# Performance work log

Hardware: AMD Instinct MI355X
Metric: run time of the kernel (lower is better)

## Reference

```python
import jax, jax.numpy as jnp
import numpy as np

B, H, S, D = 2, 8, 4096, 64
EPS = 1e-12  # torch F.normalize default eps

def _l2_normalize(x):
    n = jnp.linalg.norm(x, axis=-1, keepdims=True)
    return x / jnp.maximum(n, EPS)

def setup_inputs() -> dict:
    key = jax.random.key(0)
    kq, kk, kv, km = jax.random.split(key, 4)
    return {
        "query": jax.random.normal(kq, (B, H, S, D), dtype=jnp.float32),
        "key": jax.random.normal(kk, (B, H, S, D), dtype=jnp.float32),
        "value": jax.random.normal(kv, (B, H, S, D), dtype=jnp.float32),
        "mask": jax.random.randint(km, (B, 1, 1, S), 0, 2, dtype=jnp.int32),
    }

def reference(query, key, value, mask):
    q = _l2_normalize(query)
    k = _l2_normalize(key)
    # [B,H,S,S] cosine-similarity scores
    scores = jnp.einsum("bhqd,bhkd->bhqk", q, k)
    scores = jnp.where(mask == 0, jnp.float32(-1.0), scores)
    scores = (scores + 1.0) * 0.5  # map [-1,1] -> [0,1]; masked entries -> 0
    attention = scores / jnp.sum(scores, axis=-1, keepdims=True)
    return jnp.einsum("bhqk,bhkd->bhqd", attention, value)
```

## Files before the change

### kernel.cpp

```cpp
#include <hip/hip_runtime.h>


#define S 4096
#define D 64
#define BH 16
#define FSTRIDE 4352
#define NE 4225
#define NCHM 32
#define KSTR 36
#define QSTR 72
#define PSTR 8832
#define FTSTR 4224

typedef __attribute__((ext_vector_type(8))) short short8;
typedef __attribute__((ext_vector_type(4))) short short4v;
typedef __attribute__((ext_vector_type(4))) float f32x4;

__device__ __forceinline__ float bperm(float v, int srclane) {
    return __int_as_float(
        __builtin_amdgcn_ds_bpermute(srclane << 2, __float_as_int(v)));
}
__device__ __forceinline__ unsigned bf16h(float x) {
    unsigned u = __float_as_uint(x);
    u += 0x7FFF + ((u >> 16) & 1);
    return u >> 16;
}
__device__ __forceinline__ float bf16f(unsigned short h) {
    return __uint_as_float(((unsigned)h) << 16);
}

__global__ __launch_bounds__(256, 4) void k_moments(
    const float* __restrict__ K, const float* __restrict__ V,
    const int* __restrict__ mask, char* __restrict__ part)
{
    __shared__ unsigned short stag[8 * 64 * KSTR];
    __shared__ float sured[4 * 132];
    float* red0 = (float*)stag;
    float* red1 = red0 + 4096;

    const int tid  = threadIdx.x;
    const int lane = tid & 63;
    const int wave = tid >> 6;
    const int quad = lane >> 4;
    const int l15  = lane & 15;

    const int bh    = blockIdx.x >> 5;
    const int chunk = blockIdx.x & 31;
    const int row0  = chunk * 128 + wave * 32;

    const float* Kh = K + (size_t)bh * S * D;
    const float* Vh = V + (size_t)bh * S * D;
    const int*   mb = mask + (bh >> 3) * S;

    unsigned short* Kst = stag + wave * (64 * KSTR);
    unsigned short* Vst = stag + 4 * (64 * KSTR) + wave * (64 * KSTR);
    unsigned* KstW = (unsigned*)Kst;
    unsigned* VstW = (unsigned*)Vst;

    float4 s4 = {0.f, 0.f, 0.f, 0.f}, u4 = {0.f, 0.f, 0.f, 0.f};
    float nwp = 0.f;
    unsigned kprev[4], vprev[4];
    #pragma unroll
    for (int i = 0; i < 8; ++i) {
        const int key = 8 * quad + i;
        const int row = row0 + key;
        float4 kf = *(const float4*)(Kh + (size_t)row * D + 4 * l15);
        float4 vf = *(const float4*)(Vh + (size_t)row * D + 4 * l15);
        float ssp = kf.x * kf.x;
        ssp = fmaf(kf.y, kf.y, ssp);
        ssp = fmaf(kf.z, kf.z, ssp);
        ssp = fmaf(kf.w, kf.w, ssp);
        ssp += __shfl_xor(ssp, 1, 64);
        ssp += __shfl_xor(ssp, 2, 64);
        ssp += __shfl_xor(ssp, 4, 64);
        ssp += __shfl_xor(ssp, 8, 64);
        const float mj = (float)mb[row];
        nwp += mj;
        const float aj = mj * __builtin_amdgcn_rsqf(fmaxf(ssp, 1e-24f));
        float k0 = kf.x * aj, k1 = kf.y * aj, k2 = kf.z * aj, k3 = kf.w * aj;
        float v0 = vf.x * mj, v1 = vf.y * mj, v2 = vf.z * mj, v3 = vf.w * mj;
        s4.x += k0; s4.y += k1; s4.z += k2; s4.w += k3;
        u4.x += v0; u4.y += v1; u4.z += v2; u4.w += v3;
        unsigned kb0 = bf16h(k0), kb1 = bf16h(k1), kb2 = bf16h(k2), kb3 = bf16h(k3);
        unsigned vb0 = bf16h(v0), vb1 = bf16h(v1), vb2 = bf16h(v2), vb3 = bf16h(v3);
        if (i & 1) {
            const int base = 4 * quad + (i >> 1);
            KstW[(4 * l15 + 0) * 18 + base] = kprev[0] | (kb0 << 16);
            KstW[(4 * l15 + 1) * 18 + base] = kprev[1] | (kb1 << 16);
            KstW[(4 * l15 + 2) * 18 + base] = kprev[2] | (kb2 << 16);
            KstW[(4 * l15 + 3) * 18 + base] = kprev[3] | (kb3 << 16);
            VstW[(4 * l15 + 0) * 18 + base] = vprev[0] | (vb0 << 16);
            VstW[(4 * l15 + 1) * 18 + base] = vprev[1] | (vb1 << 16);
            VstW[(4 * l15 + 2) * 18 + base] = vprev[2] | (vb2 << 16);
            VstW[(4 * l15 + 3) * 18 + base] = vprev[3] | (vb3 << 16);
        } else {
            kprev[0] = kb0; kprev[1] = kb1; kprev[2] = kb2; kprev[3] = kb3;
            vprev[0] = vb0; vprev[1] = vb1; vprev[2] = vb2; vprev[3] = vb3;
        }
    }
    float nw = nwp;
    nw += __shfl_xor(nw, 16, 64);
    nw += __shfl_xor(nw, 32, 64);

    s4.x += __shfl_xor(s4.x, 16, 64); s4.x += __shfl_xor(s4.x, 32, 64);
    s4.y += __shfl_xor(s4.y, 16, 64); s4.y += __shfl_xor(s4.y, 32, 64);
    s4.z += __shfl_xor(s4.z, 16, 64); s4.z += __shfl_xor(s4.z, 32, 64);
    s4.w += __shfl_xor(s4.w, 16, 64); s4.w += __shfl_xor(s4.w, 32, 64);
    u4.x += __shfl_xor(u4.x, 16, 64); u4.x += __shfl_xor(u4.x, 32, 64);
    u4.y += __shfl_xor(u4.y, 16, 64); u4.y += __shfl_xor(u4.y, 32, 64);
    u4.z += __shfl_xor(u4.z, 16, 64); u4.z += __shfl_xor(u4.z, 32, 64);
    u4.w += __shfl_xor(u4.w, 16, 64); u4.w += __shfl_xor(u4.w, 32, 64);
    if (quad == 0) {
        sured[wave * 132 + 4 * l15 + 0]      = s4.x;
        sured[wave * 132 + 4 * l15 + 1]      = s4.y;
        sured[wave * 132 + 4 * l15 + 2]      = s4.z;
        sured[wave * 132 + 4 * l15 + 3]      = s4.w;
        sured[wave * 132 + 64 + 4 * l15 + 0] = u4.x;
        sured[wave * 132 + 64 + 4 * l15 + 1] = u4.y;
        sured[wave * 132 + 64 + 4 * l15 + 2] = u4.z;
        sured[wave * 132 + 64 + 4 * l15 + 3] = u4.w;
    }
    if (lane == 0) sured[wave * 132 + 128] = nw;
    __syncthreads();

    short8 af[4], bfr[4];
    #pragma unroll
    for (int t = 0; t < 4; ++t) {
        const unsigned short* ab = Kst + (t * 16 + l15) * KSTR + quad * 8;
        short4v a0 = *(const short4v*)ab;
        short4v a1 = *(const short4v*)(ab + 4);
        af[t] = __builtin_shufflevector(a0, a1, 0, 1, 2, 3, 4, 5, 6, 7);
        const unsigned short* bb = Vst + (t * 16 + l15) * KSTR + quad * 8;
        short4v b0 = *(const short4v*)bb;
        short4v b1 = *(const short4v*)(bb + 4);
        bfr[t] = __builtin_shufflevector(b0, b1, 0, 1, 2, 3, 4, 5, 6, 7);
    }
    f32x4 acc[4][4];
    #pragma unroll
    for (int tm = 0; tm < 4; ++tm)
        #pragma unroll
        for (int tn = 0; tn < 4; ++tn)
            acc[tm][tn] = (f32x4){0.f, 0.f, 0.f, 0.f};
    #pragma unroll
    for (int tn = 0; tn < 4; ++tn)
        #pragma unroll
        for (int tm = 0; tm < 4; ++tm)
            acc[tm][tn] = __builtin_amdgcn_mfma_f32_16x16x32_bf16(
                af[tm], bfr[tn], acc[tm][tn], 0, 0, 0);
    __syncthreads();

    if (wave < 2) {
        float* rd = wave ? red1 : red0;
        #pragma unroll
        for (int tm = 0; tm < 4; ++tm)
            #pragma unroll
            for (int tn = 0; tn < 4; ++tn)
                #pragma unroll
                for (int rr = 0; rr < 4; ++rr)
                    rd[(tm * 16 + quad * 4 + rr) * 64 + tn * 16 + l15]
                        = acc[tm][tn][rr];
    }
    __syncthreads();
    if (wave >= 2) {
        float* rd = (wave == 3) ? red1 : red0;
        #pragma unroll
        for (int tm = 0; tm < 4; ++tm)
            #pragma unroll
            for (int tn = 0; tn < 4; ++tn)
                #pragma unroll
                for (int rr = 0; rr < 4; ++rr)
                    rd[(tm * 16 + quad * 4 + rr) * 64 + tn * 16 + l15]
                        += acc[tm][tn][rr];
    }
    __syncthreads();

    char* pb = part + ((size_t)bh * NCHM + chunk) * PSTR;
    unsigned short* pm = (unsigned short*)pb;
    float* psu = (float*)(pb + 8192);
    for (int i = tid; i < NE; i += 256) {
        if (i < 4096)
            pm[i] = (unsigned short)bf16h(red0[i] + red1[i]);
        else {
            int e = i - 4096;
            psu[e] = sured[e] + sured[132 + e] + sured[264 + e] + sured[396 + e];
        }
    }
}

__global__ __launch_bounds__(256) void k_reduce(
    const char* __restrict__ part, float* __restrict__ fin,
    unsigned short* __restrict__ finTh)
{
    const int bh = blockIdx.x;
    const int e  = blockIdx.y * 256 + threadIdx.x;
    if (e >= NE) return;
    const char* pb = part + (size_t)bh * NCHM * PSTR;
    if (e < 4096) {
        float a0 = 0.f, a1 = 0.f, a2 = 0.f, a3 = 0.f;
        #pragma unroll
        for (int c = 0; c < NCHM; c += 4) {
            a0 += bf16f(*(const unsigned short*)(pb + (size_t)(c + 0) * PSTR + 2 * e));
            a1 += bf16f(*(const unsigned short*)(pb + (size_t)(c + 1) * PSTR + 2 * e));
            a2 += bf16f(*(const unsigned short*)(pb + (size_t)(c + 2) * PSTR + 2 * e));
            a3 += bf16f(*(const unsigned short*)(pb + (size_t)(c + 3) * PSTR + 2 * e));
        }
        float v = (a0 + a1) + (a2 + a3);
        finTh[(size_t)bh * FTSTR + (e & 63) * 64 + (e >> 6)] = (unsigned short)bf16h(v);
    } else {
        const int eo = e - 4096;
        float a0 = 0.f, a1 = 0.f, a2 = 0.f, a3 = 0.f;
        #pragma unroll
        for (int c = 0; c < NCHM; c += 4) {
            a0 += *(const float*)(pb + (size_t)(c + 0) * PSTR + 8192 + 4 * eo);
            a1 += *(const float*)(pb + (size_t)(c + 1) * PSTR + 8192 + 4 * eo);
            a2 += *(const float*)(pb + (size_t)(c + 2) * PSTR + 8192 + 4 * eo);
            a3 += *(const float*)(pb + (size_t)(c + 3) * PSTR + 8192 + 4 * eo);
        }
        float v = (a0 + a1) + (a2 + a3);
        fin[(size_t)bh * FSTRIDE + e] = v;
        if (eo < 64)
            finTh[(size_t)bh * FTSTR + 4096 + eo] = (unsigned short)bf16h(v);
    }
}

__global__ __launch_bounds__(256) void k_out(
    const float* __restrict__ Q, const float* __restrict__ fin,
    const unsigned short* __restrict__ finTh, float* __restrict__ out)
{
    __shared__ unsigned short Qst[4 * 16 * QSTR];

    const int tid  = threadIdx.x;
    const int lane = tid & 63;
    const int wave = tid >> 6;
    const int quad = lane >> 4;
    const int l15  = lane & 15;

    const int bh  = blockIdx.x >> 5;
    const int c32 = blockIdx.x & 31;

    const float* fb = fin + (size_t)bh * FSTRIDE;
    const unsigned short* fT = finTh + (size_t)bh * FTSTR;
    const float* Qh = Q + (size_t)bh * S * D;
    float*       Oh = out + (size_t)bh * S * D;

    const float nval = fb[4224];
    float uo[4];
    #pragma unroll
    for (int tn = 0; tn < 4; ++tn) uo[tn] = fb[4160 + tn * 16 + l15];

    short8 bf0[4], bf1[4];
    #pragma unroll
    for (int tn = 0; tn < 4; ++tn) {
        bf0[tn] = *(const short8*)(fT + (tn * 16 + l15) * 64 + quad * 8);
        bf1[tn] = *(const short8*)(fT + (tn * 16 + l15) * 64 + 32 + quad * 8);
    }
    short8 sz = {0, 0, 0, 0, 0, 0, 0, 0};
    short8 sv0 = *(const short8*)(fT + 4096 + quad * 8);
    short8 sv1 = *(const short8*)(fT + 4096 + 32 + quad * 8);
    short8 bs0 = (l15 == 0) ? sv0 : sz;
    short8 bs1 = (l15 == 0) ? sv1 : sz;

    unsigned short* Qw = Qst + wave * 16 * QSTR;

    #pragma unroll
    for (int cc = 0; cc < 2; ++cc) {
        const int row0w = (c32 * 2 + cc) * 64 + wave * 16;

        #pragma unroll
        for (int i = 0; i < 4; ++i) {
            const int r = 4 * quad + i;
            float4 qv = *(const float4*)(Qh + (size_t)(row0w + r) * D + 4 * l15);
            float ssp = qv.x * qv.x;
            ssp = fmaf(qv.y, qv.y, ssp);
            ssp = fmaf(qv.z, qv.z, ssp);
            ssp = fmaf(qv.w, qv.w, ssp);
            ssp += __shfl_xor(ssp, 1, 64);
            ssp += __shfl_xor(ssp, 2, 64);
            ssp += __shfl_xor(ssp, 4, 64);
            ssp += __shfl_xor(ssp, 8, 64);
            const float iq = __builtin_amdgcn_rsqf(fmaxf(ssp, 1e-24f));
            unsigned b0 = bf16h(qv.x * iq), b1 = bf16h(qv.y * iq);
            unsigned b2 = bf16h(qv.z * iq), b3 = bf16h(qv.w * iq);
            uint2 w; w.x = b0 | (b1 << 16); w.y = b2 | (b3 << 16);
            *(uint2*)(Qw + r * QSTR + 4 * l15) = w;
        }
        asm volatile("" ::: "memory");

        short8 af0 = *(const short8*)(Qw + l15 * QSTR + quad * 8);
        short8 af1 = *(const short8*)(Qw + l15 * QSTR + 32 + quad * 8);

        f32x4 acc[4], acc5;
        #pragma unroll
        for (int tn = 0; tn < 4; ++tn) acc[tn] = (f32x4){0.f, 0.f, 0.f, 0.f};
        acc5 = (f32x4){0.f, 0.f, 0.f, 0.f};
        #pragma unroll
        for (int tn = 0; tn < 4; ++tn) {
            acc[tn] = __builtin_amdgcn_mfma_f32_16x16x32_bf16(af0, bf0[tn], acc[tn], 0, 0, 0);
            acc[tn] = __builtin_amdgcn_mfma_f32_16x16x32_bf16(af1, bf1[tn], acc[tn], 0, 0, 0);
        }
        acc5 = __builtin_amdgcn_mfma_f32_16x16x32_bf16(af0, bs0, acc5, 0, 0, 0);
        acc5 = __builtin_amdgcn_mfma_f32_16x16x32_bf16(af1, bs1, acc5, 0, 0, 0);

        #pragma unroll
        for (int rr = 0; rr < 4; ++rr) {
            float den = bperm(acc5[rr], 16 * quad) + nval;
            float rd = 1.f / den;
            const size_t row = row0w + quad * 4 + rr;
            #pragma unroll
            for (int tn = 0; tn < 4; ++tn)
                Oh[row * D + tn * 16 + l15] = (acc[tn][rr] + uo[tn]) * rd;
        }
        asm volatile("" ::: "memory");
    }
}

extern "C" void kernel_launch(void* const* d_in, const int* in_sizes, int n_in,
                              void* d_out, int out_size, void* d_ws, size_t ws_size,
                              hipStream_t stream) {
    const float* Q    = (const float*)d_in[0];
    const float* K    = (const float*)d_in[1];
    const float* V    = (const float*)d_in[2];
    const int*   mask = (const int*)d_in[3];
    float* out = (float*)d_out;
    char*  ws  = (char*)d_ws;

    float*          fin   = (float*)ws;
    unsigned short* finTh = (unsigned short*)(ws + (size_t)BH * FSTRIDE * 4);
    char*           part  = (char*)finTh + (size_t)BH * FTSTR * 2;

    k_moments<<<dim3(512), 256, 0, stream>>>(K, V, mask, part);
    k_reduce <<<dim3(BH, (NE + 255) / 256), 256, 0, stream>>>(part, fin, finTh);
    k_out    <<<dim3(512), 256, 0, stream>>>(Q, fin, finTh, out);
}
```

Measured before the change: 105.1 us.

## Double waves in moments kernel, double out-kernel grid, use packed bf16 convert

k_moments now runs 512 threads per block, with pairs of waves each loading half of a 32-row slice. Only the first four waves then run the MFMA outer product, and the column-sum reduction covers eight waves. k_out launches 1024 blocks, each handling a single 64-row chunk instead of looping over two. Manual bf16 rounding is replaced by the v_cvt_pk_bf16_f32 instruction. The aim is more memory-level parallelism and occupancy for the load-bound phases, at the cost of idle waves during the MFMA phase and higher per-block overhead.

```diff
diff --git a/kernel.cpp b/kernel.cpp
--- a/kernel.cpp
+++ b/kernel.cpp
@@ -28,13 +28,18 @@
 __device__ __forceinline__ float bf16f(unsigned short h) {
     return __uint_as_float(((unsigned)h) << 16);
 }
-
-__global__ __launch_bounds__(256, 4) void k_moments(
+__device__ __forceinline__ unsigned cvt_pk_bf16(float a, float b) {
+    unsigned r;
+    asm("v_cvt_pk_bf16_f32 %0, %1, %2" : "=v"(r) : "v"(a), "v"(b));
+    return r;
+}
+
+__global__ __launch_bounds__(512, 4) void k_moments(
     const float* __restrict__ K, const float* __restrict__ V,
     const int* __restrict__ mask, char* __restrict__ part)
 {
     __shared__ unsigned short stag[8 * 64 * KSTR];
-    __shared__ float sured[4 * 132];
+    __shared__ float sured[8 * 132];
     float* red0 = (float*)stag;
     float* red1 = red0 + 4096;
 
@@ -43,27 +48,28 @@
     const int wave = tid >> 6;
     const int quad = lane >> 4;
     const int l15  = lane & 15;
+    const int pair = wave >> 1;
+    const int half = wave & 1;
 
     const int bh    = blockIdx.x >> 5;
     const int chunk = blockIdx.x & 31;
-    const int row0  = chunk * 128 + wave * 32;
+    const int row0  = chunk * 128 + pair * 32 + half * 16;
 
     const float* Kh = K + (size_t)bh * S * D;
     const float* Vh = V + (size_t)bh * S * D;
     const int*   mb = mask + (bh >> 3) * S;
 
-    unsigned short* Kst = stag + wave * (64 * KSTR);
-    unsigned short* Vst = stag + 4 * (64 * KSTR) + wave * (64 * KSTR);
+    unsigned short* Kst = stag + pair * (64 * KSTR);
+    unsigned short* Vst = stag + 4 * (64 * KSTR) + pair * (64 * KSTR);
     unsigned* KstW = (unsigned*)Kst;
     unsigned* VstW = (unsigned*)Vst;
 
     float4 s4 = {0.f, 0.f, 0.f, 0.f}, u4 = {0.f, 0.f, 0.f, 0.f};
     float nwp = 0.f;
-    unsigned kprev[4], vprev[4];
-    #pragma unroll
-    for (int i = 0; i < 8; ++i) {
-        const int key = 8 * quad + i;
-        const int row = row0 + key;
+    float kprev[4], vprev[4];
+    #pragma unroll
+    for (int i = 0; i < 4; ++i) {
+        const int row = row0 + 4 * quad + i;
         float4 kf = *(const float4*)(Kh + (size_t)row * D + 4 * l15);
         float4 vf = *(const float4*)(Vh + (size_t)row * D + 4 * l15);
         float ssp = kf.x * kf.x;
@@ -81,21 +87,19 @@
         float v0 = vf.x * mj, v1 = vf.y * mj, v2 = vf.z * mj, v3 = vf.w * mj;
         s4.x += k0; s4.y += k1; s4.z += k2; s4.w += k3;
         u4.x += v0; u4.y += v1; u4.z += v2; u4.w += v3;
-        unsigned kb0 = bf16h(k0), kb1 = bf16h(k1), kb2 = bf16h(k2), kb3 = bf16h(k3);
-        unsigned vb0 = bf16h(v0), vb1 = bf16h(v1), vb2 = bf16h(v2), vb3 = bf16h(v3);
         if (i & 1) {
-            const int base = 4 * quad + (i >> 1);
-            KstW[(4 * l15 + 0) * 18 + base] = kprev[0] | (kb0 << 16);
-            KstW[(4 * l15 + 1) * 18 + base] = kprev[1] | (kb1 << 16);
-            KstW[(4 * l15 + 2) * 18 + base] = kprev[2] | (kb2 << 16);
-            KstW[(4 * l15 + 3) * 18 + base] = kprev[3] | (kb3 << 16);
-            VstW[(4 * l15 + 0) * 18 + base] = vprev[0] | (vb0 << 16);
-            VstW[(4 * l15 + 1) * 18 + base] = vprev[1] | (vb1 << 16);
-            VstW[(4 * l15 + 2) * 18 + base] = vprev[2] | (vb2 << 16);
-            VstW[(4 * l15 + 3) * 18 + base] = vprev[3] | (vb3 << 16);
+            const int base = 8 * half + 2 * quad + (i >> 1);
+            KstW[(4 * l15 + 0) * 18 + base] = cvt_pk_bf16(kprev[0], k0);
+            KstW[(4 * l15 + 1) * 18 + base] = cvt_pk_bf16(kprev[1], k1);
+            KstW[(4 * l15 + 2) * 18 + base] = cvt_pk_bf16(kprev[2], k2);
+            KstW[(4 * l15 + 3) * 18 + base] = cvt_pk_bf16(kprev[3], k3);
+            VstW[(4 * l15 + 0) * 18 + base] = cvt_pk_bf16(vprev[0], v0);
+            VstW[(4 * l15 + 1) * 18 + base] = cvt_pk_bf16(vprev[1], v1);
+            VstW[(4 * l15 + 2) * 18 + base] = cvt_pk_bf16(vprev[2], v2);
+            VstW[(4 * l15 + 3) * 18 + base] = cvt_pk_bf16(vprev[3], v3);
         } else {
-            kprev[0] = kb0; kprev[1] = kb1; kprev[2] = kb2; kprev[3] = kb3;
-            vprev[0] = vb0; vprev[1] = vb1; vprev[2] = vb2; vprev[3] = vb3;
+            kprev[0] = k0; kprev[1] = k1; kprev[2] = k2; kprev[3] = k3;
+            vprev[0] = v0; vprev[1] = v1; vprev[2] = v2; vprev[3] = v3;
         }
     }
     float nw = nwp;
@@ -123,30 +127,34 @@
     if (lane == 0) sured[wave * 132 + 128] = nw;
     __syncthreads();
 
-    short8 af[4], bfr[4];
-    #pragma unroll
-    for (int t = 0; t < 4; ++t) {
-        const unsigned short* ab = Kst + (t * 16 + l15) * KSTR + quad * 8;
-        short4v a0 = *(const short4v*)ab;
-        short4v a1 = *(const short4v*)(ab + 4);
-        af[t] = __builtin_shufflevector(a0, a1, 0, 1, 2, 3, 4, 5, 6, 7);
-        const unsigned short* bb = Vst + (t * 16 + l15) * KSTR + quad * 8;
-        short4v b0 = *(const short4v*)bb;
-        short4v b1 = *(const short4v*)(bb + 4);
-        bfr[t] = __builtin_shufflevector(b0, b1, 0, 1, 2, 3, 4, 5, 6, 7);
-    }
     f32x4 acc[4][4];
-    #pragma unroll
-    for (int tm = 0; tm < 4; ++tm)
+    if (wave < 4) {
+        const unsigned short* Kr = stag + wave * (64 * KSTR);
+        const unsigned short* Vr = stag + 4 * (64 * KSTR) + wave * (64 * KSTR);
+        short8 af[4], bfr[4];
+        #pragma unroll
+        for (int t = 0; t < 4; ++t) {
+            const unsigned short* ab = Kr + (t * 16 + l15) * KSTR + quad * 8;
+            short4v a0 = *(const short4v*)ab;
+            short4v a1 = *(const short4v*)(ab + 4);
+            af[t] = __builtin_shufflevector(a0, a1, 0, 1, 2, 3, 4, 5, 6, 7);
+            const unsigned short* bb = Vr + (t * 16 + l15) * KSTR + quad * 8;
+            short4v b0 = *(const short4v*)bb;
+            short4v b1 = *(const short4v*)(bb + 4);
+            bfr[t] = __builtin_shufflevector(b0, b1, 0, 1, 2, 3, 4, 5, 6, 7);
+        }
+        #pragma unroll
+        for (int tm = 0; tm < 4; ++tm)
+            #pragma unroll
+            for (int tn = 0; tn < 4; ++tn)
+                acc[tm][tn] = (f32x4){0.f, 0.f, 0.f, 0.f};
         #pragma unroll
         for (int tn = 0; tn < 4; ++tn)
-            acc[tm][tn] = (f32x4){0.f, 0.f, 0.f, 0.f};
-    #pragma unroll
-    for (int tn = 0; tn < 4; ++tn)
-        #pragma unroll
-        for (int tm = 0; tm < 4; ++tm)
-            acc[tm][tn] = __builtin_amdgcn_mfma_f32_16x16x32_bf16(
-                af[tm], bfr[tn], acc[tm][tn], 0, 0, 0);
+            #pragma unroll
+            for (int tm = 0; tm < 4; ++tm)
+                acc[tm][tn] = __builtin_amdgcn_mfma_f32_16x16x32_bf16(
+                    af[tm], bfr[tn], acc[tm][tn], 0, 0, 0);
+    }
     __syncthreads();
 
     if (wave < 2) {
@@ -161,7 +169,7 @@
                         = acc[tm][tn][rr];
     }
     __syncthreads();
-    if (wave >= 2) {
+    if (wave == 2 || wave == 3) {
         float* rd = (wave == 3) ? red1 : red0;
         #pragma unroll
         for (int tm = 0; tm < 4; ++tm)
@@ -177,12 +185,15 @@
     char* pb = part + ((size_t)bh * NCHM + chunk) * PSTR;
     unsigned short* pm = (unsigned short*)pb;
     float* psu = (float*)(pb + 8192);
-    for (int i = tid; i < NE; i += 256) {
+    for (int i = tid; i < NE; i += 512) {
         if (i < 4096)
             pm[i] = (unsigned short)bf16h(red0[i] + red1[i]);
         else {
             int e = i - 4096;
-            psu[e] = sured[e] + sured[132 + e] + sured[264 + e] + sured[396 + e];
+            float v = 0.f;
+            #pragma unroll
+            for (int w = 0; w < 8; ++w) v += sured[w * 132 + e];
+            psu[e] = v;
         }
     }
 }
@@ -235,8 +246,8 @@
     const int quad = lane >> 4;
     const int l15  = lane & 15;
 
-    const int bh  = blockIdx.x >> 5;
-    const int c32 = blockIdx.x & 31;
+    const int bh  = blockIdx.x >> 6;
+    const int c64 = blockIdx.x & 63;
 
     const float* fb = fin + (size_t)bh * FSTRIDE;
     const unsigned short* fT = finTh + (size_t)bh * FTSTR;
@@ -261,56 +272,51 @@
     short8 bs1 = (l15 == 0) ? sv1 : sz;
 
     unsigned short* Qw = Qst + wave * 16 * QSTR;
-
-    #pragma unroll
-    for (int cc = 0; cc < 2; ++cc) {
-        const int row0w = (c32 * 2 + cc) * 64 + wave * 16;
-
-        #pragma unroll
-        for (int i = 0; i < 4; ++i) {
-            const int r = 4 * quad + i;
-            float4 qv = *(const float4*)(Qh + (size_t)(row0w + r) * D + 4 * l15);
-            float ssp = qv.x * qv.x;
-            ssp = fmaf(qv.y, qv.y, ssp);
-            ssp = fmaf(qv.z, qv.z, ssp);
-            ssp = fmaf(qv.w, qv.w, ssp);
-            ssp += __shfl_xor(ssp, 1, 64);
-            ssp += __shfl_xor(ssp, 2, 64);
-            ssp += __shfl_xor(ssp, 4, 64);
-            ssp += __shfl_xor(ssp, 8, 64);
-            const float iq = __builtin_amdgcn_rsqf(fmaxf(ssp, 1e-24f));
-            unsigned b0 = bf16h(qv.x * iq), b1 = bf16h(qv.y * iq);
-            unsigned b2 = bf16h(qv.z * iq), b3 = bf16h(qv.w * iq);
-            uint2 w; w.x = b0 | (b1 << 16); w.y = b2 | (b3 << 16);
-            *(uint2*)(Qw + r * QSTR + 4 * l15) = w;
-        }
-        asm volatile("" ::: "memory");
-
-        short8 af0 = *(const short8*)(Qw + l15 * QSTR + quad * 8);
-        short8 af1 = *(const short8*)(Qw + l15 * QSTR + 32 + quad * 8);
-
-        f32x4 acc[4], acc5;
-        #pragma unroll
-        for (int tn = 0; tn < 4; ++tn) acc[tn] = (f32x4){0.f, 0.f, 0.f, 0.f};
-        acc5 = (f32x4){0.f, 0.f, 0.f, 0.f};
-        #pragma unroll
-        for (int tn = 0; tn < 4; ++tn) {
-            acc[tn] = __builtin_amdgcn_mfma_f32_16x16x32_bf16(af0, bf0[tn], acc[tn], 0, 0, 0);
-            acc[tn] = __builtin_amdgcn_mfma_f32_16x16x32_bf16(af1, bf1[tn], acc[tn], 0, 0, 0);
-        }
-        acc5 = __builtin_amdgcn_mfma_f32_16x16x32_bf16(af0, bs0, acc5, 0, 0, 0);
-        acc5 = __builtin_amdgcn_mfma_f32_16x16x32_bf16(af1, bs1, acc5, 0, 0, 0);
-
-        #pragma unroll
-        for (int rr = 0; rr < 4; ++rr) {
-            float den = bperm(acc5[rr], 16 * quad) + nval;
-            float rd = 1.f / den;
-            const size_t row = row0w + quad * 4 + rr;
-            #pragma unroll
-            for (int tn = 0; tn < 4; ++tn)
-                Oh[row * D + tn * 16 + l15] = (acc[tn][rr] + uo[tn]) * rd;
-        }
-        asm volatile("" ::: "memory");
+    const int row0w = c64 * 64 + wave * 16;
+
+    #pragma unroll
+    for (int i = 0; i < 4; ++i) {
+        const int r = 4 * quad + i;
+        float4 qv = *(const float4*)(Qh + (size_t)(row0w + r) * D + 4 * l15);
+        float ssp = qv.x * qv.x;
+        ssp = fmaf(qv.y, qv.y, ssp);
+        ssp = fmaf(qv.z, qv.z, ssp);
+        ssp = fmaf(qv.w, qv.w, ssp);
+        ssp += __shfl_xor(ssp, 1, 64);
+        ssp += __shfl_xor(ssp, 2, 64);
+        ssp += __shfl_xor(ssp, 4, 64);
+        ssp += __shfl_xor(ssp, 8, 64);
+        const float iq = __builtin_amdgcn_rsqf(fmaxf(ssp, 1e-24f));
+        uint2 w;
+        w.x = cvt_pk_bf16(qv.x * iq, qv.y * iq);
+        w.y = cvt_pk_bf16(qv.z * iq, qv.w * iq);
+        *(uint2*)(Qw + r * QSTR + 4 * l15) = w;
+    }
+    asm volatile("" ::: "memory");
+
+    short8 af0 = *(const short8*)(Qw + l15 * QSTR + quad * 8);
+    short8 af1 = *(const short8*)(Qw + l15 * QSTR + 32 + quad * 8);
+
+    f32x4 acc[4], acc5;
+    #pragma unroll
+    for (int tn = 0; tn < 4; ++tn) acc[tn] = (f32x4){0.f, 0.f, 0.f, 0.f};
+    acc5 = (f32x4){0.f, 0.f, 0.f, 0.f};
+    #pragma unroll
+    for (int tn = 0; tn < 4; ++tn) {
+        acc[tn] = __builtin_amdgcn_mfma_f32_16x16x32_bf16(af0, bf0[tn], acc[tn], 0, 0, 0);
+        acc[tn] = __builtin_amdgcn_mfma_f32_16x16x32_bf16(af1, bf1[tn], acc[tn], 0, 0, 0);
+    }
+    acc5 = __builtin_amdgcn_mfma_f32_16x16x32_bf16(af0, bs0, acc5, 0, 0, 0);
+    acc5 = __builtin_amdgcn_mfma_f32_16x16x32_bf16(af1, bs1, acc5, 0, 0, 0);
+
+    #pragma unroll
+    for (int rr = 0; rr < 4; ++rr) {
+        float den = bperm(acc5[rr], 16 * quad) + nval;
+        float rd = 1.f / den;
+        const size_t row = row0w + quad * 4 + rr;
+        #pragma unroll
+        for (int tn = 0; tn < 4; ++tn)
+            Oh[row * D + tn * 16 + l15] = (acc[tn][rr] + uo[tn]) * rd;
     }
 }
 
@@ -328,7 +334,7 @@
     unsigned short* finTh = (unsigned short*)(ws + (size_t)BH * FSTRIDE * 4);
     char*           part  = (char*)finTh + (size_t)BH * FTSTR * 2;
 
-    k_moments<<<dim3(512), 256, 0, stream>>>(K, V, mask, part);
+    k_moments<<<dim3(512), 512, 0, stream>>>(K, V, mask, part);
     k_reduce <<<dim3(BH, (NE + 255) / 256), 256, 0, stream>>>(part, fin, finTh);
-    k_out    <<<dim3(512), 256, 0, stream>>>(Q, fin, finTh, out);
-}
+    k_out    <<<dim3(1024), 256, 0, stream>>>(Q, fin, finTh, out);
+}
```

Measured after the change: 105.1 us. About the same (+0.0%).
